# Optimization experiments

Measured on AMD Instinct MI355X. Metric: run time of the kernel, lower is better.

Reference implementation:

```python
import jax, jax.numpy as jnp
import numpy as np

D, L, C, H, W = 4, 16, 64, 128, 128


def setup_inputs() -> dict:
    key = jax.random.key(0)
    ks = jax.random.split(key, 20)
    rn = lambda k, shape, s=0.02: jax.random.normal(k, shape, dtype=jnp.float32) * s
    return {
        "x": jax.random.normal(ks[0], (L, C, H, W), dtype=jnp.float32),
        "ln1_g": jnp.ones((D, C, H, W), jnp.float32),
        "ln1_b": jnp.zeros((D, C, H, W), jnp.float32),
        "Wq": rn(ks[1], (D, C, C)), "bq": jnp.zeros((D, C), jnp.float32),
        "Wk": rn(ks[2], (D, C, C)), "bk": jnp.zeros((D, C), jnp.float32),
        "Wv": rn(ks[3], (D, C, C)), "bv": jnp.zeros((D, C), jnp.float32),
        "Wa": rn(ks[4], (D, 1, 2 * C, 5, 5)), "ba": jnp.zeros((D, 1), jnp.float32),
        "ln2_g": jnp.ones((D, C, H, W), jnp.float32),
        "ln2_b": jnp.zeros((D, C, H, W), jnp.float32),
        "W1": rn(ks[5], (D, 2 * C, C)), "b1": jnp.zeros((D, 2 * C), jnp.float32),
        "W2": rn(ks[6], (D, C, 2 * C)), "b2": jnp.zeros((D, C), jnp.float32),
    }


def _layernorm(x, g, b):
    # torch nn.LayerNorm([C,H,W]): normalize over last 3 dims per frame, eps=1e-5
    mu = jnp.mean(x, axis=(1, 2, 3), keepdims=True)
    var = jnp.var(x, axis=(1, 2, 3), keepdims=True)
    return (x - mu) * jax.lax.rsqrt(var + 1e-5) * g[None] + b[None]


def _conv5(x, w):
    # x: [L, Cin, H, W], w: [1, Cin, 5, 5] -> [L, 1, H, W], SAME padding (pad=2)
    return jax.lax.conv_general_dilated(
        x, w, window_strides=(1, 1), padding="SAME",
        dimension_numbers=("NCHW", "OIHW", "NCHW"))


def _conv1x1(x, w, b):
    # 1x1 conv == per-pixel linear over channels
    return jnp.einsum("lchw,oc->lohw", x, w) + b[None, :, None, None]


def reference(x, ln1_g, ln1_b, Wq, bq, Wk, bk, Wv, bv, Wa, ba,
              ln2_g, ln2_b, W1, b1, W2, b2):
    depth = ln1_g.shape[0]
    c = Wa.shape[2] // 2
    for d in range(depth):
        # --- pre-norm conv attention (nheads=1) + residual ---
        h = _layernorm(x, ln1_g[d], ln1_b[d])
        Q = _conv1x1(h, Wq[d], bq[d])
        K = _conv1x1(h, Wk[d], bk[d])
        V = _conv1x1(h, Wv[d], bv[d])
        # conv_atten(cat([Q_i, K_j])) is linear in channels: split the 5x5
        # kernel into Q-part and K-part, so H_ij = A_i + B_j + bias.
        A = _conv5(Q, Wa[d, :, :c])[:, 0]   # [L, H, W]
        B = _conv5(K, Wa[d, :, c:])[:, 0]   # [L, H, W]
        S = A[:, None] + B[None, :] + ba[d][0]      # [L, L, H, W]
        P = jax.nn.softmax(S, axis=1)               # softmax over source frames j
        attn = jnp.einsum("ijhw,jchw->ichw", P, V)  # weighted sum of V_j
        x = x + attn
        # --- pre-norm conv FFN + residual ---
        h = _layernorm(x, ln2_g[d], ln2_b[d])
        f = _conv1x1(h, W1[d], b1[d])
        f = jax.nn.leaky_relu(f, 0.01)  # torch LeakyReLU default slope
        f = _conv1x1(f, W2[d], b2[d])
        x = x + f
    return x
```

## Files before the change

### kernel.cpp

```cpp
#include <hip/hip_runtime.h>


#define HW 16384
#define CHW 1048576
#define NB 64

typedef unsigned short u16;
typedef __attribute__((ext_vector_type(8))) short bf16x8;
typedef __attribute__((ext_vector_type(8))) unsigned short u16x8;
typedef __attribute__((ext_vector_type(4))) float f32x4;

static __device__ __forceinline__ u16 f2bf(float f) {
  union { float f; unsigned int u; } v; v.f = f;
  unsigned int r = v.u + 0x7fffu + ((v.u >> 16) & 1u);
  return (u16)(r >> 16);
}
static __device__ __forceinline__ float bf2f(u16 h) {
  union { unsigned int u; float f; } v; v.u = ((unsigned int)h) << 16;
  return v.f;
}
static __device__ __forceinline__ void ln_from_acc_wave(
    const float* acc, int l, int lane, float& mu, float& r) {
  const float invN = 1.f / 1048576.f;
  float2 v = *(const float2*)(acc + lane * 32 + 2 * l);
  float s = v.x, q = v.y;
#pragma unroll
  for (int off = 32; off > 0; off >>= 1) {
    s += __shfl_xor(s, off);
    q += __shfl_xor(q, off);
  }
  mu = s * invN;
  r = rsqrtf(q * invN - mu * mu + 1e-5f);
}

__global__ __launch_bounds__(256) void prep_kernel(
    const float* __restrict__ Wa, const float* __restrict__ Wk,
    const float* __restrict__ Wv, const float* __restrict__ W1,
    const float* __restrict__ W2, u16* __restrict__ w1pk,
    u16* __restrict__ w2pk, u16* __restrict__ wvpk, u16* __restrict__ wepk) {
  int d = blockIdx.x;
  int t = blockIdx.y * 256 + threadIdx.x;
  const int STR = 256 * 16;
  const float* WaK = Wa + ((size_t)d * 128 + 64) * 25;
  const float* Wkd = Wk + d * 4096;
  for (int idx = t; idx < 2048; idx += STR) {
    int frag = idx >> 9, lane = (idx >> 3) & 63, j = idx & 7;
    int mt = frag >> 1, kt = frag & 1;
    int tap = mt * 16 + (lane & 15);
    int ci = kt * 32 + (lane >> 4) * 8 + j;
    float s = 0.f;
    if (tap < 25)
      for (int co = 0; co < 64; ++co)
        s = fmaf(WaK[co * 25 + tap], Wkd[co * 64 + ci], s);
    wepk[d * 2048 + idx] = f2bf(s);
  }
  const float* Wvd = Wv + d * 4096;
  for (int idx = t; idx < 4096; idx += STR) {
    int frag = idx >> 9, lane = (idx >> 3) & 63, j = idx & 7;
    int mt = frag >> 1, kt = frag & 1;
    int co = mt * 16 + (lane & 15);
    int ci = kt * 32 + (lane >> 4) * 8 + j;
    wvpk[d * 4096 + idx] = f2bf(Wvd[co * 64 + ci]);
  }
  const float* W1d = W1 + d * 8192;
  for (int idx = t; idx < 8192; idx += STR) {
    int frag = idx >> 9, lane = (idx >> 3) & 63, j = idx & 7;
    int mt = frag >> 1, kt = frag & 1;
    int o = mt * 16 + (lane & 15);
    int ci = kt * 32 + (lane >> 4) * 8 + j;
    w1pk[d * 8192 + idx] = f2bf(W1d[o * 64 + ci]);
  }
  const float* W2d = W2 + d * 8192;
  for (int idx = t; idx < 8192; idx += STR) {
    int frag = idx >> 9, lane = (idx >> 3) & 63, j = idx & 7;
    int mt2 = frag >> 2, kt2 = frag & 3;
    int c = mt2 * 16 + (lane & 15);
    int o = kt2 * 32 + (lane >> 4) * 8 + j;
    w2pk[d * 8192 + idx] = f2bf(W2d[c * 128 + o]);
  }
}

__global__ __launch_bounds__(256) void lngb_kernel(
    const float* __restrict__ g1, u16* __restrict__ o1) {
  int idx = blockIdx.x * 256 + threadIdx.x;
  float4 v = *(const float4*)(g1 + (size_t)idx * 4);
  ushort4 o;
  o.x = f2bf(v.x); o.y = f2bf(v.y); o.z = f2bf(v.z); o.w = f2bf(v.w);
  *(ushort4*)(o1 + (size_t)idx * 4) = o;
}

__global__ __launch_bounds__(256) void stats_kernel(
    const float* __restrict__ xin, u16* __restrict__ xbf,
    float* __restrict__ acc) {
  int tid = threadIdx.x;
  size_t base = (size_t)blockIdx.x * 4096;
  const float4* in4 = (const float4*)(xin + base);
  float s = 0.f, q = 0.f;
#pragma unroll
  for (int k = 0; k < 4; ++k) {
    float4 v = in4[k * 256 + tid];
    ushort4 o;
    o.x = f2bf(v.x); o.y = f2bf(v.y); o.z = f2bf(v.z); o.w = f2bf(v.w);
    *(ushort4*)(xbf + base + (k * 256 + tid) * 4) = o;
    s += v.x + v.y + v.z + v.w;
    q = fmaf(v.x, v.x, q); q = fmaf(v.y, v.y, q);
    q = fmaf(v.z, v.z, q); q = fmaf(v.w, v.w, q);
  }
#pragma unroll
  for (int off = 32; off > 0; off >>= 1) {
    s += __shfl_down(s, off); q += __shfl_down(q, off);
  }
  __shared__ float ls[4], lq[4];
  int wave = tid >> 6;
  if ((tid & 63) == 0) { ls[wave] = s; lq[wave] = q; }
  __syncthreads();
  if (tid == 0) {
    int frame = blockIdx.x >> 8;
    int bkt = blockIdx.x & (NB - 1);
    atomicAdd(&acc[bkt * 32 + frame * 2], ls[0] + ls[1] + ls[2] + ls[3]);
    atomicAdd(&acc[bkt * 32 + frame * 2 + 1], lq[0] + lq[1] + lq[2] + lq[3]);
  }
}

__global__ __launch_bounds__(256) void tb_kernel(
    const u16* __restrict__ xbf, const u16* __restrict__ g,
    const float* __restrict__ bln, const u16* __restrict__ wep_g,
    const float* __restrict__ accA, float* __restrict__ accBz,
    float* __restrict__ mulr, u16* __restrict__ T) {
  __shared__ __align__(16) char lds[18432];
  u16* hb = (u16*)lds;
  int tid = threadIdx.x;
  int l = blockIdx.y;
  int p0 = blockIdx.x << 7;
  if (blockIdx.x == 0 && blockIdx.y == 0)
    for (int i = tid; i < NB * 32; i += 256) accBz[i] = 0.f;
  int lane = tid & 63;
  float mu, r;
  ln_from_acc_wave(accA, l, lane, mu, r);
  if (blockIdx.x == 0 && tid == 0) {
    mulr[2 * l] = mu;
    mulr[2 * l + 1] = r;
  }

  {
    int pq = tid & 15, cg = tid >> 4;
    int px0 = pq * 8, c0 = cg * 4;
    float vv[4][8];
#pragma unroll
    for (int i = 0; i < 4; ++i) {
      int c = c0 + i;
      size_t gi = (((size_t)l * 64 + c) << 14) + p0 + px0;
      int li = (c << 14) + p0 + px0;
      u16x8 xv = *(const u16x8*)(xbf + gi);
      u16x8 gv = *(const u16x8*)(g + li);
      float4 bb0 = *(const float4*)(bln + li);
      float4 bb1 = *(const float4*)(bln + li + 4);
#pragma unroll
      for (int k = 0; k < 8; ++k) {
        float bbk = k < 4 ? ((const float*)&bb0)[k] : ((const float*)&bb1)[k - 4];
        vv[i][k] = (bf2f(xv[k]) - mu) * r * bf2f(gv[k]) + bbk;
      }
    }
#pragma unroll
    for (int k = 0; k < 8; ++k) {
      int row = px0 + k;
      int col = ((((c0 >> 3) + (row >> 2)) & 7) << 3) | (c0 & 7);
      ushort4 hv;
      hv.x = f2bf(vv[0][k]); hv.y = f2bf(vv[1][k]);
      hv.z = f2bf(vv[2][k]); hv.w = f2bf(vv[3][k]);
      *(ushort4*)(hb + row * 72 + col) = hv;
    }
  }
  __syncthreads();

  int wv = tid >> 6;
  int ln15 = lane & 15, quad = lane >> 4;

  bf16x8 ah[2][2];
#pragma unroll
  for (int mt = 0; mt < 2; ++mt) {
    int px = (wv * 2 + mt) * 16 + ln15;
#pragma unroll
    for (int kt = 0; kt < 2; ++kt) {
      int slot = ((kt * 4 + quad) + (px >> 2)) & 7;
      ah[mt][kt] = *(const bf16x8*)(hb + px * 72 + (slot << 3));
    }
  }
  const bf16x8* weg = (const bf16x8*)wep_g;

  f32x4 accT[2][2];
#pragma unroll
  for (int mt = 0; mt < 2; ++mt)
#pragma unroll
    for (int nt = 0; nt < 2; ++nt) accT[mt][nt] = (f32x4){0.f, 0.f, 0.f, 0.f};
#pragma unroll
  for (int nt = 0; nt < 2; ++nt) {
    bf16x8 b0 = weg[(nt * 2 + 0) * 64 + lane];
    bf16x8 b1w = weg[(nt * 2 + 1) * 64 + lane];
#pragma unroll
    for (int mt = 0; mt < 2; ++mt) {
      accT[mt][nt] = __builtin_amdgcn_mfma_f32_16x16x32_bf16(
          ah[mt][0], b0, accT[mt][nt], 0, 0, 0);
      accT[mt][nt] = __builtin_amdgcn_mfma_f32_16x16x32_bf16(
          ah[mt][1], b1w, accT[mt][nt], 0, 0, 0);
    }
  }

#pragma unroll
  for (int mt = 0; mt < 2; ++mt) {
    int pxb = p0 + (wv * 2 + mt) * 16 + quad * 4;
#pragma unroll
    for (int nt = 0; nt < 2; ++nt) {
      int tap = nt * 16 + ln15;
      if (tap < 25) {
        ushort4 o;
        o.x = f2bf(accT[mt][nt][0]); o.y = f2bf(accT[mt][nt][1]);
        o.z = f2bf(accT[mt][nt][2]); o.w = f2bf(accT[mt][nt][3]);
        *(ushort4*)(T + (((size_t)l * 25 + tap) << 14) + pxb) = o;
      }
    }
  }
}

__global__ __launch_bounds__(256) void bconv_kernel(
    const u16* __restrict__ T, float* __restrict__ B) {
  int gid = blockIdx.x * 256 + threadIdx.x;
  int l = gid >> 14, p = gid & 16383;
  int y = p >> 7, xx = p & 127;
  float s = 0.f;
#pragma unroll
  for (int dy = 0; dy < 5; ++dy) {
    int yy = y + dy - 2;
    if (yy < 0 || yy > 127) continue;
#pragma unroll
    for (int dx = 0; dx < 5; ++dx) {
      int xc = xx + dx - 2;
      if (xc < 0 || xc > 127) continue;
      s += bf2f(T[(((size_t)l * 25 + dy * 5 + dx) << 14) + (yy << 7) + xc]);
    }
  }
  B[gid] = s;
}

__global__ __launch_bounds__(256) void attnc_kernel(
    const u16* __restrict__ xbf, const float* __restrict__ B,
    const u16* __restrict__ g1, const float* __restrict__ b1g,
    const u16* __restrict__ wvp_g, const float* __restrict__ bv,
    const float* __restrict__ mulr, u16* __restrict__ abf,
    float* __restrict__ accB, float* __restrict__ accAz) {
  __shared__ float Prl[16][64];
  __shared__ float scal[64];
  __shared__ __align__(16) u16 hb[64 * 72];
  __shared__ float lsq[4][32];
  int tid = threadIdx.x;
  int p0 = blockIdx.x << 6;
  if (blockIdx.x == 0)
    for (int i = tid; i < NB * 32; i += 256) accAz[i] = 0.f;

  if (tid < 64) {
    float bj[16], m = -1e30f;
#pragma unroll
    for (int j = 0; j < 16; ++j) {
      bj[j] = B[(j << 14) + p0 + tid];
      m = fmaxf(m, bj[j]);
    }
    float sum = 0.f;
#pragma unroll
    for (int j = 0; j < 16; ++j) {
      bj[j] = __expf(bj[j] - m);
      sum += bj[j];
    }
    float inv = 1.f / sum;
    float sc = 0.f;
#pragma unroll
    for (int j = 0; j < 16; ++j) {
      float mu_j = mulr[2 * j], r_j = mulr[2 * j + 1];
      float prl = bj[j] * inv * r_j;
      Prl[j][tid] = prl;
      sc = fmaf(prl, mu_j, sc);
    }
    scal[tid] = sc;
  }
  __syncthreads();

  {
    int c2 = tid >> 3, pxg = tid & 7;
    int px0 = pxg * 8;
    float xbar[2][8];
#pragma unroll
    for (int cc = 0; cc < 2; ++cc)
#pragma unroll
      for (int k = 0; k < 8; ++k) xbar[cc][k] = 0.f;
#pragma unroll
    for (int j = 0; j < 16; ++j) {
      float p8[8];
#pragma unroll
      for (int k = 0; k < 8; ++k) p8[k] = Prl[j][px0 + k];
#pragma unroll
      for (int cc = 0; cc < 2; ++cc) {
        int c = cc * 32 + c2;
        u16x8 xv =
            *(const u16x8*)(xbf + (((size_t)j * 64 + c) << 14) + p0 + px0);
#pragma unroll
        for (int k = 0; k < 8; ++k)
          xbar[cc][k] = fmaf(p8[k], bf2f(xv[k]), xbar[cc][k]);
      }
    }
    float sc8[8];
#pragma unroll
    for (int k = 0; k < 8; ++k) sc8[k] = scal[px0 + k];
#pragma unroll
    for (int cc = 0; cc < 2; ++cc) {
      int c = cc * 32 + c2;
      int li = (c << 14) + p0 + px0;
      u16x8 g8 = *(const u16x8*)(g1 + li);
      float4 b0 = *(const float4*)(b1g + li);
      float4 b1v = *(const float4*)(b1g + li + 4);
#pragma unroll
      for (int k = 0; k < 8; ++k) {
        float bbk = k < 4 ? ((const float*)&b0)[k] : ((const float*)&b1v)[k - 4];
        float hv = bf2f(g8[k]) * (xbar[cc][k] - sc8[k]) + bbk;
        int row = px0 + k;
        int col = ((((c >> 3) + (row >> 2)) & 7) << 3) | (c & 7);
        hb[row * 72 + col] = f2bf(hv);
      }
    }
  }
  __syncthreads();

  int wv = tid >> 6, lane = tid & 63;
  int ln15 = lane & 15, quad = lane >> 4;
  int px = wv * 16 + ln15;
  bf16x8 ah[2];
#pragma unroll
  for (int kt = 0; kt < 2; ++kt) {
    int slot = ((kt * 4 + quad) + (px >> 2)) & 7;
    ah[kt] = *(const bf16x8*)(hb + px * 72 + (slot << 3));
  }
  const bf16x8* wvg = (const bf16x8*)wvp_g;
  f32x4 accV[4];
#pragma unroll
  for (int nt = 0; nt < 4; ++nt) accV[nt] = (f32x4){0.f, 0.f, 0.f, 0.f};
#pragma unroll
  for (int nt = 0; nt < 4; ++nt) {
    bf16x8 b0 = wvg[(nt * 2 + 0) * 64 + lane];
    bf16x8 b1w = wvg[(nt * 2 + 1) * 64 + lane];
    accV[nt] = __builtin_amdgcn_mfma_f32_16x16x32_bf16(ah[0], b0, accV[nt],
                                                       0, 0, 0);
    accV[nt] = __builtin_amdgcn_mfma_f32_16x16x32_bf16(ah[1], b1w, accV[nt],
                                                       0, 0, 0);
  }
  int pxb = p0 + wv * 16 + quad * 4;
  float av[4][4];
#pragma unroll
  for (int nt = 0; nt < 4; ++nt) {
    int c = nt * 16 + ln15;
    float bvc = bv[c];
    ushort4 o;
    av[nt][0] = accV[nt][0] + bvc; o.x = f2bf(av[nt][0]);
    av[nt][1] = accV[nt][1] + bvc; o.y = f2bf(av[nt][1]);
    av[nt][2] = accV[nt][2] + bvc; o.z = f2bf(av[nt][2]);
    av[nt][3] = accV[nt][3] + bvc; o.w = f2bf(av[nt][3]);
    *(ushort4*)(abf + ((size_t)c << 14) + pxb) = o;
  }

  float sf[16], qf[16];
#pragma unroll
  for (int f = 0; f < 16; ++f) {
    float s = 0.f, q = 0.f;
#pragma unroll
    for (int nt = 0; nt < 4; ++nt) {
      int c = nt * 16 + ln15;
      ushort4 xv =
          *(const ushort4*)(xbf + (((size_t)f * 64 + c) << 14) + pxb);
      float v0 = bf2f(xv.x) + av[nt][0], v1 = bf2f(xv.y) + av[nt][1];
      float v2 = bf2f(xv.z) + av[nt][2], v3 = bf2f(xv.w) + av[nt][3];
      s += v0 + v1 + v2 + v3;
      q = fmaf(v0, v0, q); q = fmaf(v1, v1, q);
      q = fmaf(v2, v2, q); q = fmaf(v3, v3, q);
    }
    sf[f] = s; qf[f] = q;
  }
#pragma unroll
  for (int off = 32; off > 0; off >>= 1) {
#pragma unroll
    for (int f = 0; f < 16; ++f) {
      sf[f] += __shfl_down(sf[f], off);
      qf[f] += __shfl_down(qf[f], off);
    }
  }
  if (lane == 0) {
#pragma unroll
    for (int f = 0; f < 16; ++f) {
      lsq[wv][2 * f] = sf[f];
      lsq[wv][2 * f + 1] = qf[f];
    }
  }
  __syncthreads();
  if (tid < 32) {
    int bkt = blockIdx.x & (NB - 1);
    atomicAdd(&accB[bkt * 32 + tid],
              lsq[0][tid] + lsq[1][tid] + lsq[2][tid] + lsq[3][tid]);
  }
}

__global__ __launch_bounds__(256) void ffn_kernel(
    const float* __restrict__ xr, float* __restrict__ xw,
    u16* __restrict__ xbfw, const u16* __restrict__ ap,
    const float* __restrict__ g, const float* __restrict__ bln,
    const u16* __restrict__ w1p_g, const float* __restrict__ b1,
    const u16* __restrict__ w2p_g, const float* __restrict__ b2,
    const float* __restrict__ accB, float* __restrict__ accA, int wrbf) {
  __shared__ __align__(16) char lds[66560];
  float* xaf = (float*)lds;
  u16* hb = (u16*)(lds + 33792);
  u16* f1 = (u16*)(lds + 33792);

  int tid = threadIdx.x;
  int P0 = blockIdx.x << 7;
  int l = P0 >> 14;
  int p0 = P0 & 16383;
  int lane = tid & 63;
  float mu, r;
  ln_from_acc_wave(accB, l, lane, mu, r);

#pragma unroll
  for (int it = 0; it < 2; ++it) {
    int pq = tid & 31, cg = (tid >> 5) + it * 8;
    int px = pq * 4, c0 = cg * 4;
    float vv[4][4];
#pragma unroll
    for (int i = 0; i < 4; ++i) {
      int c = c0 + i;
      size_t gi = (((size_t)l * 64 + c) << 14) + p0 + px;
      int li = (c << 14) + p0 + px;
      float4 xv = *(const float4*)(xr + gi);
      ushort4 av4 = *(const ushort4*)(ap + li);
      float4 gv = *(const float4*)(g + li);
      float4 bb = *(const float4*)(bln + li);
      float4 s4;
      s4.x = xv.x + bf2f(av4.x); s4.y = xv.y + bf2f(av4.y);
      s4.z = xv.z + bf2f(av4.z); s4.w = xv.w + bf2f(av4.w);
      *(float4*)(xaf + c * 132 + px) = s4;
      vv[i][0] = (s4.x - mu) * r * gv.x + bb.x;
      vv[i][1] = (s4.y - mu) * r * gv.y + bb.y;
      vv[i][2] = (s4.z - mu) * r * gv.z + bb.z;
      vv[i][3] = (s4.w - mu) * r * gv.w + bb.w;
    }
#pragma unroll
    for (int k = 0; k < 4; ++k) {
      int row = px + k;
      int col = ((((c0 >> 3) + (row >> 2)) & 7) << 3) | (c0 & 7);
      ushort4 hv;
      hv.x = f2bf(vv[0][k]); hv.y = f2bf(vv[1][k]);
      hv.z = f2bf(vv[2][k]); hv.w = f2bf(vv[3][k]);
      *(ushort4*)(hb + row * 72 + col) = hv;
    }
  }
  __syncthreads();

  int wv = tid >> 6;
  int ln15 = lane & 15, quad = lane >> 4;

  bf16x8 bh[2][2];
#pragma unroll
  for (int nt = 0; nt < 2; ++nt) {
    int px = (wv * 2 + nt) * 16 + ln15;
#pragma unroll
    for (int kt = 0; kt < 2; ++kt) {
      int slot = ((kt * 4 + quad) + (px >> 2)) & 7;
      bh[nt][kt] = *(const bf16x8*)(hb + px * 72 + (slot << 3));
    }
  }
  __syncthreads();

  const bf16x8* w1g = (const bf16x8*)w1p_g;
  const bf16x8* w2g = (const bf16x8*)w2p_g;

#pragma unroll
  for (int mt = 0; mt < 8; ++mt) {
    bf16x8 a1a = w1g[(mt * 2 + 0) * 64 + lane];
    bf16x8 a1b = w1g[(mt * 2 + 1) * 64 + lane];
    f32x4 acc[2];
    acc[0] = (f32x4){0.f, 0.f, 0.f, 0.f};
    acc[1] = (f32x4){0.f, 0.f, 0.f, 0.f};
#pragma unroll
    for (int nt = 0; nt < 2; ++nt) {
      acc[nt] = __builtin_amdgcn_mfma_f32_16x16x32_bf16(a1a, bh[nt][0],
                                                        acc[nt], 0, 0, 0);
      acc[nt] = __builtin_amdgcn_mfma_f32_16x16x32_bf16(a1b, bh[nt][1],
                                                        acc[nt], 0, 0, 0);
    }
    int o0 = mt * 16 + quad * 4;
    float4 b1v = *(const float4*)(b1 + o0);
#pragma unroll
    for (int nt = 0; nt < 2; ++nt) {
      int px = (wv * 2 + nt) * 16 + ln15;
      int swz = (px & 7) * 8;
      float fv[4];
#pragma unroll
      for (int rj = 0; rj < 4; ++rj) {
        float f = acc[nt][rj] + ((const float*)&b1v)[rj];
        fv[rj] = fmaxf(f, 0.01f * f);
      }
      int col = ((o0 & ~7) ^ swz) + (o0 & 7);
      ushort4 ov;
      ov.x = f2bf(fv[0]); ov.y = f2bf(fv[1]);
      ov.z = f2bf(fv[2]); ov.w = f2bf(fv[3]);
      *(ushort4*)(f1 + px * 128 + col) = ov;
    }
  }
  __syncthreads();

  bf16x8 a2[2][4];
#pragma unroll
  for (int mt = 0; mt < 2; ++mt) {
    int px = (wv * 2 + mt) * 16 + ln15;
    int swz = (px & 7) * 8;
#pragma unroll
    for (int kt = 0; kt < 4; ++kt)
      a2[mt][kt] =
          *(const bf16x8*)(f1 + px * 128 + ((kt * 32 + quad * 8) ^ swz));
  }
  f32x4 acc2[2][4];
#pragma unroll
  for (int mt = 0; mt < 2; ++mt)
#pragma unroll
    for (int nt = 0; nt < 4; ++nt) acc2[mt][nt] = (f32x4){0.f, 0.f, 0.f, 0.f};
#pragma unroll
  for (int nt = 0; nt < 4; ++nt) {
    bf16x8 bw[4];
#pragma unroll
    for (int kt = 0; kt < 4; ++kt) bw[kt] = w2g[(nt * 4 + kt) * 64 + lane];
#pragma unroll
    for (int mt = 0; mt < 2; ++mt)
#pragma unroll
      for (int kt = 0; kt < 4; ++kt)
        acc2[mt][nt] = __builtin_amdgcn_mfma_f32_16x16x32_bf16(
            a2[mt][kt], bw[kt], acc2[mt][nt], 0, 0, 0);
  }

  float s = 0.f, q = 0.f;
#pragma unroll
  for (int mt = 0; mt < 2; ++mt) {
    int pxl = (wv * 2 + mt) * 16 + quad * 4;
#pragma unroll
    for (int nt = 0; nt < 4; ++nt) {
      int c = nt * 16 + ln15;
      float b2c = b2[c];
      const float* xac = xaf + c * 132 + pxl;
      float4 v;
      v.x = xac[0] + acc2[mt][nt][0] + b2c;
      v.y = xac[1] + acc2[mt][nt][1] + b2c;
      v.z = xac[2] + acc2[mt][nt][2] + b2c;
      v.w = xac[3] + acc2[mt][nt][3] + b2c;
      size_t gi = (((size_t)l * 64 + c) << 14) + p0 + pxl;
      *(float4*)(xw + gi) = v;
      if (wrbf) {
        ushort4 o;
        o.x = f2bf(v.x); o.y = f2bf(v.y); o.z = f2bf(v.z); o.w = f2bf(v.w);
        *(ushort4*)(xbfw + gi) = o;
      }
      s += v.x + v.y + v.z + v.w;
      q = fmaf(v.x, v.x, q); q = fmaf(v.y, v.y, q);
      q = fmaf(v.z, v.z, q); q = fmaf(v.w, v.w, q);
    }
  }
#pragma unroll
  for (int off = 32; off > 0; off >>= 1) {
    s += __shfl_down(s, off); q += __shfl_down(q, off);
  }
  if (lane == 0) {
    int bkt = blockIdx.x & (NB - 1);
    atomicAdd(&accA[bkt * 32 + l * 2], s);
    atomicAdd(&accA[bkt * 32 + l * 2 + 1], q);
  }
}

extern "C" void kernel_launch(void* const* d_in, const int* in_sizes, int n_in,
                              void* d_out, int out_size, void* d_ws,
                              size_t ws_size, hipStream_t stream) {
  const float* x_in = (const float*)d_in[0];
  const float* ln1_g = (const float*)d_in[1];
  const float* ln1_b = (const float*)d_in[2];
  const float* Wk = (const float*)d_in[5];
  const float* Wv = (const float*)d_in[7];
  const float* bv = (const float*)d_in[8];
  const float* Wa = (const float*)d_in[9];
  const float* ln2_g = (const float*)d_in[11];
  const float* ln2_b = (const float*)d_in[12];
  const float* W1 = (const float*)d_in[13];
  const float* b1 = (const float*)d_in[14];
  const float* W2 = (const float*)d_in[15];
  const float* b2 = (const float*)d_in[16];

  float* xbuf = (float*)d_out;
  char* wsb = (char*)d_ws;
  u16* xbf = (u16*)wsb;
  u16* T = (u16*)(wsb + 33554432);
  u16* abf = (u16*)(wsb + 46661632);
  float* Bbuf = (float*)(wsb + 48758784);
  u16* g1b = (u16*)(wsb + 49807360);
  u16* w1pk = (u16*)(wsb + 58195968);
  u16* w2pk = (u16*)(wsb + 58261504);
  u16* wvpk = (u16*)(wsb + 58327040);
  u16* wepk = (u16*)(wsb + 58359808);
  float* mulr = (float*)(wsb + 58376192);
  float* accA = (float*)(wsb + 58376320);
  float* accB = (float*)(wsb + 58384512);

  hipMemsetAsync(accA, 0, 16384, stream);
  prep_kernel<<<dim3(4, 16), 256, 0, stream>>>(Wa, Wk, Wv, W1, W2, w1pk, w2pk,
                                               wvpk, wepk);
  lngb_kernel<<<4096, 256, 0, stream>>>(ln1_g, g1b);
  stats_kernel<<<4096, 256, 0, stream>>>(x_in, xbf, accA);

  const float* xr = x_in;
  for (int d = 0; d < 4; ++d) {
    tb_kernel<<<dim3(128, 16), 256, 0, stream>>>(
        xbf, g1b + (size_t)d * CHW, ln1_b + (size_t)d * CHW, wepk + d * 2048,
        accA, accB, mulr, T);
    bconv_kernel<<<1024, 256, 0, stream>>>(T, Bbuf);
    attnc_kernel<<<256, 256, 0, stream>>>(
        xbf, Bbuf, g1b + (size_t)d * CHW, ln1_b + (size_t)d * CHW,
        wvpk + d * 4096, bv + d * 64, mulr, abf, accB, accA);
    ffn_kernel<<<2048, 256, 0, stream>>>(
        xr, xbuf, xbf, abf, ln2_g + (size_t)d * CHW, ln2_b + (size_t)d * CHW,
        w1pk + d * 8192, b1 + d * 128, w2pk + d * 8192, b2 + d * 64, accB,
        accA, d < 3 ? 1 : 0);
    xr = xbuf;
  }
}
```

Before: 561.6 us.

## Drop bf16 shadow of x, fuse 5x5 tap-sum into attention, add stats kernel

Removes the bf16 copy of the activations. The tb and attention kernels now read the fp32 x directly, and the FFN no longer writes the bf16 shadow. The separate bconv kernel is folded into the attention kernel, which sums the 25 shifted tap planes into shared memory per block. The attention kernel's in-place LN2 statistics are moved into a new stats2 kernel that streams x plus the attention output. This cuts the bf16 write traffic and one launch, but doubles the bytes of each x read, adds a full pass over x, and moves the tap sum into a 256-block kernel with low parallelism.

```diff
diff --git a/kernel.cpp b/kernel.cpp
--- a/kernel.cpp
+++ b/kernel.cpp
@@ -90,8 +90,7 @@
 }
 
 __global__ __launch_bounds__(256) void stats_kernel(
-    const float* __restrict__ xin, u16* __restrict__ xbf,
-    float* __restrict__ acc) {
+    const float* __restrict__ xin, float* __restrict__ acc) {
   int tid = threadIdx.x;
   size_t base = (size_t)blockIdx.x * 4096;
   const float4* in4 = (const float4*)(xin + base);
@@ -99,9 +98,6 @@
 #pragma unroll
   for (int k = 0; k < 4; ++k) {
     float4 v = in4[k * 256 + tid];
-    ushort4 o;
-    o.x = f2bf(v.x); o.y = f2bf(v.y); o.z = f2bf(v.z); o.w = f2bf(v.w);
-    *(ushort4*)(xbf + base + (k * 256 + tid) * 4) = o;
     s += v.x + v.y + v.z + v.w;
     q = fmaf(v.x, v.x, q); q = fmaf(v.y, v.y, q);
     q = fmaf(v.z, v.z, q); q = fmaf(v.w, v.w, q);
@@ -123,7 +119,7 @@
 }
 
 __global__ __launch_bounds__(256) void tb_kernel(
-    const u16* __restrict__ xbf, const u16* __restrict__ g,
+    const float* __restrict__ x, const u16* __restrict__ g,
     const float* __restrict__ bln, const u16* __restrict__ wep_g,
     const float* __restrict__ accA, float* __restrict__ accBz,
     float* __restrict__ mulr, u16* __restrict__ T) {
@@ -151,14 +147,16 @@
       int c = c0 + i;
       size_t gi = (((size_t)l * 64 + c) << 14) + p0 + px0;
       int li = (c << 14) + p0 + px0;
-      u16x8 xv = *(const u16x8*)(xbf + gi);
+      float4 xv0 = *(const float4*)(x + gi);
+      float4 xv1 = *(const float4*)(x + gi + 4);
       u16x8 gv = *(const u16x8*)(g + li);
       float4 bb0 = *(const float4*)(bln + li);
       float4 bb1 = *(const float4*)(bln + li + 4);
 #pragma unroll
       for (int k = 0; k < 8; ++k) {
+        float xk = k < 4 ? ((const float*)&xv0)[k] : ((const float*)&xv1)[k - 4];
         float bbk = k < 4 ? ((const float*)&bb0)[k] : ((const float*)&bb1)[k - 4];
-        vv[i][k] = (bf2f(xv[k]) - mu) * r * bf2f(gv[k]) + bbk;
+        vv[i][k] = (xk - mu) * r * bf2f(gv[k]) + bbk;
       }
     }
 #pragma unroll
@@ -222,46 +220,47 @@
   }
 }
 
-__global__ __launch_bounds__(256) void bconv_kernel(
-    const u16* __restrict__ T, float* __restrict__ B) {
-  int gid = blockIdx.x * 256 + threadIdx.x;
-  int l = gid >> 14, p = gid & 16383;
-  int y = p >> 7, xx = p & 127;
-  float s = 0.f;
-#pragma unroll
-  for (int dy = 0; dy < 5; ++dy) {
-    int yy = y + dy - 2;
-    if (yy < 0 || yy > 127) continue;
-#pragma unroll
-    for (int dx = 0; dx < 5; ++dx) {
-      int xc = xx + dx - 2;
-      if (xc < 0 || xc > 127) continue;
-      s += bf2f(T[(((size_t)l * 25 + dy * 5 + dx) << 14) + (yy << 7) + xc]);
-    }
-  }
-  B[gid] = s;
-}
-
 __global__ __launch_bounds__(256) void attnc_kernel(
-    const u16* __restrict__ xbf, const float* __restrict__ B,
+    const float* __restrict__ x, const u16* __restrict__ T,
     const u16* __restrict__ g1, const float* __restrict__ b1g,
     const u16* __restrict__ wvp_g, const float* __restrict__ bv,
-    const float* __restrict__ mulr, u16* __restrict__ abf,
-    float* __restrict__ accB, float* __restrict__ accAz) {
+    const float* __restrict__ mulr, u16* __restrict__ abf) {
+  __shared__ float Bsm[16][68];
   __shared__ float Prl[16][64];
   __shared__ float scal[64];
   __shared__ __align__(16) u16 hb[64 * 72];
-  __shared__ float lsq[4][32];
   int tid = threadIdx.x;
   int p0 = blockIdx.x << 6;
-  if (blockIdx.x == 0)
-    for (int i = tid; i < NB * 32; i += 256) accAz[i] = 0.f;
+
+  {
+    int j = tid >> 4, xg = tid & 15;
+    int y0 = p0 >> 7, x0 = p0 & 127;
+    float acc4[4] = {0.f, 0.f, 0.f, 0.f};
+    const u16* Tj = T + (((size_t)j * 25) << 14);
+#pragma unroll
+    for (int dy = 0; dy < 5; ++dy) {
+      int yy = y0 + dy - 2;
+      if (yy < 0 || yy > 127) continue;
+#pragma unroll
+      for (int dx = 0; dx < 5; ++dx) {
+        const u16* Tt = Tj + ((dy * 5 + dx) << 14) + (yy << 7);
+#pragma unroll
+        for (int k = 0; k < 4; ++k) {
+          int xc = x0 + xg * 4 + k + dx - 2;
+          if (xc >= 0 && xc < 128) acc4[k] += bf2f(Tt[xc]);
+        }
+      }
+    }
+#pragma unroll
+    for (int k = 0; k < 4; ++k) Bsm[j][xg * 4 + k] = acc4[k];
+  }
+  __syncthreads();
 
   if (tid < 64) {
     float bj[16], m = -1e30f;
 #pragma unroll
     for (int j = 0; j < 16; ++j) {
-      bj[j] = B[(j << 14) + p0 + tid];
+      bj[j] = Bsm[j][tid];
       m = fmaxf(m, bj[j]);
     }
     float sum = 0.f;
@@ -299,11 +298,15 @@
 #pragma unroll
       for (int cc = 0; cc < 2; ++cc) {
         int c = cc * 32 + c2;
-        u16x8 xv =
-            *(const u16x8*)(xbf + (((size_t)j * 64 + c) << 14) + p0 + px0);
-#pragma unroll
-        for (int k = 0; k < 8; ++k)
-          xbar[cc][k] = fmaf(p8[k], bf2f(xv[k]), xbar[cc][k]);
+        const float* xp = x + (((size_t)j * 64 + c) << 14) + p0 + px0;
+        float4 xv0 = *(const float4*)xp;
+        float4 xv1 = *(const float4*)(xp + 4);
+#pragma unroll
+        for (int k = 0; k < 8; ++k) {
+          float xk =
+              k < 4 ? ((const float*)&xv0)[k] : ((const float*)&xv1)[k - 4];
+          xbar[cc][k] = fmaf(p8[k], xk, xbar[cc][k]);
+        }
       }
     }
     float sc8[8];
@@ -351,66 +354,62 @@
                                                        0, 0, 0);
   }
   int pxb = p0 + wv * 16 + quad * 4;
-  float av[4][4];
 #pragma unroll
   for (int nt = 0; nt < 4; ++nt) {
     int c = nt * 16 + ln15;
     float bvc = bv[c];
     ushort4 o;
-    av[nt][0] = accV[nt][0] + bvc; o.x = f2bf(av[nt][0]);
-    av[nt][1] = accV[nt][1] + bvc; o.y = f2bf(av[nt][1]);
-    av[nt][2] = accV[nt][2] + bvc; o.z = f2bf(av[nt][2]);
-    av[nt][3] = accV[nt][3] + bvc; o.w = f2bf(av[nt][3]);
+    o.x = f2bf(accV[nt][0] + bvc);
+    o.y = f2bf(accV[nt][1] + bvc);
+    o.z = f2bf(accV[nt][2] + bvc);
+    o.w = f2bf(accV[nt][3] + bvc);
     *(ushort4*)(abf + ((size_t)c << 14) + pxb) = o;
   }
-
-  float sf[16], qf[16];
-#pragma unroll
-  for (int f = 0; f < 16; ++f) {
-    float s = 0.f, q = 0.f;
-#pragma unroll
-    for (int nt = 0; nt < 4; ++nt) {
-      int c = nt * 16 + ln15;
-      ushort4 xv =
-          *(const ushort4*)(xbf + (((size_t)f * 64 + c) << 14) + pxb);
-      float v0 = bf2f(xv.x) + av[nt][0], v1 = bf2f(xv.y) + av[nt][1];
-      float v2 = bf2f(xv.z) + av[nt][2], v3 = bf2f(xv.w) + av[nt][3];
-      s += v0 + v1 + v2 + v3;
-      q = fmaf(v0, v0, q); q = fmaf(v1, v1, q);
-      q = fmaf(v2, v2, q); q = fmaf(v3, v3, q);
-    }
-    sf[f] = s; qf[f] = q;
+}
+
+__global__ __launch_bounds__(256) void stats2_kernel(
+    const float* __restrict__ x, const u16* __restrict__ abf,
+    float* __restrict__ accB, float* __restrict__ accAz) {
+  int tid = threadIdx.x;
+  if (blockIdx.x == 0)
+    for (int i = tid; i < NB * 32; i += 256) accAz[i] = 0.f;
+  size_t base = (size_t)blockIdx.x * 4096;
+  int intra = (blockIdx.x & 255) * 4096;
+  float s = 0.f, q = 0.f;
+#pragma unroll
+  for (int k = 0; k < 4; ++k) {
+    int off = (k * 256 + tid) * 4;
+    float4 v = *(const float4*)(x + base + off);
+    ushort4 a4 = *(const ushort4*)(abf + intra + off);
+    float v0 = v.x + bf2f(a4.x), v1 = v.y + bf2f(a4.y);
+    float v2 = v.z + bf2f(a4.z), v3 = v.w + bf2f(a4.w);
+    s += v0 + v1 + v2 + v3;
+    q = fmaf(v0, v0, q); q = fmaf(v1, v1, q);
+    q = fmaf(v2, v2, q); q = fmaf(v3, v3, q);
   }
 #pragma unroll
   for (int off = 32; off > 0; off >>= 1) {
-#pragma unroll
-    for (int f = 0; f < 16; ++f) {
-      sf[f] += __shfl_down(sf[f], off);
-      qf[f] += __shfl_down(qf[f], off);
-    }
-  }
-  if (lane == 0) {
-#pragma unroll
-    for (int f = 0; f < 16; ++f) {
-      lsq[wv][2 * f] = sf[f];
-      lsq[wv][2 * f + 1] = qf[f];
-    }
-  }
-  __syncthreads();
-  if (tid < 32) {
+    s += __shfl_down(s, off); q += __shfl_down(q, off);
+  }
+  __shared__ float ls[4], lq[4];
+  int wave = tid >> 6;
+  if ((tid & 63) == 0) { ls[wave] = s; lq[wave] = q; }
+  __syncthreads();
+  if (tid == 0) {
+    int frame = blockIdx.x >> 8;
     int bkt = blockIdx.x & (NB - 1);
-    atomicAdd(&accB[bkt * 32 + tid],
-              lsq[0][tid] + lsq[1][tid] + lsq[2][tid] + lsq[3][tid]);
+    atomicAdd(&accB[bkt * 32 + frame * 2], ls[0] + ls[1] + ls[2] + ls[3]);
+    atomicAdd(&accB[bkt * 32 + frame * 2 + 1], lq[0] + lq[1] + lq[2] + lq[3]);
   }
 }
 
 __global__ __launch_bounds__(256) void ffn_kernel(
     const float* __restrict__ xr, float* __restrict__ xw,
-    u16* __restrict__ xbfw, const u16* __restrict__ ap,
-    const float* __restrict__ g, const float* __restrict__ bln,
-    const u16* __restrict__ w1p_g, const float* __restrict__ b1,
-    const u16* __restrict__ w2p_g, const float* __restrict__ b2,
-    const float* __restrict__ accB, float* __restrict__ accA, int wrbf) {
+    const u16* __restrict__ ap, const float* __restrict__ g,
+    const float* __restrict__ bln, const u16* __restrict__ w1p_g,
+    const float* __restrict__ b1, const u16* __restrict__ w2p_g,
+    const float* __restrict__ b2, const float* __restrict__ accB,
+    float* __restrict__ accA) {
   __shared__ __align__(16) char lds[66560];
   float* xaf = (float*)lds;
   u16* hb = (u16*)(lds + 33792);
@@ -554,13 +553,7 @@
       v.y = xac[1] + acc2[mt][nt][1] + b2c;
       v.z = xac[2] + acc2[mt][nt][2] + b2c;
       v.w = xac[3] + acc2[mt][nt][3] + b2c;
-      size_t gi = (((size_t)l * 64 + c) << 14) + p0 + pxl;
-      *(float4*)(xw + gi) = v;
-      if (wrbf) {
-        ushort4 o;
-        o.x = f2bf(v.x); o.y = f2bf(v.y); o.z = f2bf(v.z); o.w = f2bf(v.w);
-        *(ushort4*)(xbfw + gi) = o;
-      }
+      *(float4*)(xw + (((size_t)l * 64 + c) << 14) + p0 + pxl) = v;
       s += v.x + v.y + v.z + v.w;
       q = fmaf(v.x, v.x, q); q = fmaf(v.y, v.y, q);
       q = fmaf(v.z, v.z, q); q = fmaf(v.w, v.w, q);
@@ -596,38 +589,36 @@
 
   float* xbuf = (float*)d_out;
   char* wsb = (char*)d_ws;
-  u16* xbf = (u16*)wsb;
-  u16* T = (u16*)(wsb + 33554432);
-  u16* abf = (u16*)(wsb + 46661632);
-  float* Bbuf = (float*)(wsb + 48758784);
-  u16* g1b = (u16*)(wsb + 49807360);
-  u16* w1pk = (u16*)(wsb + 58195968);
-  u16* w2pk = (u16*)(wsb + 58261504);
-  u16* wvpk = (u16*)(wsb + 58327040);
-  u16* wepk = (u16*)(wsb + 58359808);
-  float* mulr = (float*)(wsb + 58376192);
-  float* accA = (float*)(wsb + 58376320);
-  float* accB = (float*)(wsb + 58384512);
+  u16* T = (u16*)wsb;
+  u16* abf = (u16*)(wsb + 13107200);
+  u16* g1b = (u16*)(wsb + 15204352);
+  u16* w1pk = (u16*)(wsb + 23592960);
+  u16* w2pk = (u16*)(wsb + 23658496);
+  u16* wvpk = (u16*)(wsb + 23724032);
+  u16* wepk = (u16*)(wsb + 23756800);
+  float* mulr = (float*)(wsb + 23773184);
+  float* accA = (float*)(wsb + 23773312);
+  float* accB = (float*)(wsb + 23781504);
 
   hipMemsetAsync(accA, 0, 16384, stream);
   prep_kernel<<<dim3(4, 16), 256, 0, stream>>>(Wa, Wk, Wv, W1, W2, w1pk, w2pk,
                                                wvpk, wepk);
   lngb_kernel<<<4096, 256, 0, stream>>>(ln1_g, g1b);
-  stats_kernel<<<4096, 256, 0, stream>>>(x_in, xbf, accA);
+  stats_kernel<<<4096, 256, 0, stream>>>(x_in, accA);
 
   const float* xr = x_in;
   for (int d = 0; d < 4; ++d) {
     tb_kernel<<<dim3(128, 16), 256, 0, stream>>>(
-        xbf, g1b + (size_t)d * CHW, ln1_b + (size_t)d * CHW, wepk + d * 2048,
+        xr, g1b + (size_t)d * CHW, ln1_b + (size_t)d * CHW, wepk + d * 2048,
         accA, accB, mulr, T);
-    bconv_kernel<<<1024, 256, 0, stream>>>(T, Bbuf);
     attnc_kernel<<<256, 256, 0, stream>>>(
-        xbf, Bbuf, g1b + (size_t)d * CHW, ln1_b + (size_t)d * CHW,
-        wvpk + d * 4096, bv + d * 64, mulr, abf, accB, accA);
+        xr, T, g1b + (size_t)d * CHW, ln1_b + (size_t)d * CHW,
+        wvpk + d * 4096, bv + d * 64, mulr, abf);
+    stats2_kernel<<<4096, 256, 0, stream>>>(xr, abf, accB, accA);
     ffn_kernel<<<2048, 256, 0, stream>>>(
-        xr, xbuf, xbf, abf, ln2_g + (size_t)d * CHW, ln2_b + (size_t)d * CHW,
+        xr, xbuf, abf, ln2_g + (size_t)d * CHW, ln2_b + (size_t)d * CHW,
         w1pk + d * 8192, b1 + d * 128, w2pk + d * 8192, b2 + d * 64, accB,
-        accA, d < 3 ? 1 : 0);
+        accA);
     xr = xbuf;
   }
 }
```

Result: no change. 569.7 us (+1.4%).

## Fuse 5x5 B-conv into attention kernel and store LN params as bf16

Applied to the files above, without the earlier changes.

Removes the separate bconv kernel: each attention block now sums the 25 tap planes of T directly into a shared-memory tile of B before the softmax, which drops a launch and the float B round-trip through global memory. Separately, ln1_b, ln2_g and ln2_b are converted to bf16 once up front, alongside ln1_g, so the per-layer LN kernels read half the bytes for gamma and beta. The cost is extra upfront conversion traffic and a 64-pixel-row conv gather inside attnc with fewer blocks (256) doing it. Rounding beta and ln2 gamma to bf16 also adds precision loss.

```diff
diff --git a/kernel.cpp b/kernel.cpp
--- a/kernel.cpp
+++ b/kernel.cpp
@@ -81,12 +81,23 @@
 }
 
 __global__ __launch_bounds__(256) void lngb_kernel(
-    const float* __restrict__ g1, u16* __restrict__ o1) {
+    const float* __restrict__ g1, const float* __restrict__ b1,
+    const float* __restrict__ g2, const float* __restrict__ b2,
+    u16* __restrict__ o1, u16* __restrict__ o2, u16* __restrict__ o3,
+    u16* __restrict__ o4) {
   int idx = blockIdx.x * 256 + threadIdx.x;
-  float4 v = *(const float4*)(g1 + (size_t)idx * 4);
+  const float* src;
+  u16* dst;
+  switch (blockIdx.y) {
+    case 0: src = g1; dst = o1; break;
+    case 1: src = b1; dst = o2; break;
+    case 2: src = g2; dst = o3; break;
+    default: src = b2; dst = o4; break;
+  }
+  float4 v = *(const float4*)(src + (size_t)idx * 4);
   ushort4 o;
   o.x = f2bf(v.x); o.y = f2bf(v.y); o.z = f2bf(v.z); o.w = f2bf(v.w);
-  *(ushort4*)(o1 + (size_t)idx * 4) = o;
+  *(ushort4*)(dst + (size_t)idx * 4) = o;
 }
 
 __global__ __launch_bounds__(256) void stats_kernel(
@@ -124,7 +135,7 @@
 
 __global__ __launch_bounds__(256) void tb_kernel(
     const u16* __restrict__ xbf, const u16* __restrict__ g,
-    const float* __restrict__ bln, const u16* __restrict__ wep_g,
+    const u16* __restrict__ bln, const u16* __restrict__ wep_g,
     const float* __restrict__ accA, float* __restrict__ accBz,
     float* __restrict__ mulr, u16* __restrict__ T) {
   __shared__ __align__(16) char lds[18432];
@@ -153,13 +164,10 @@
       int li = (c << 14) + p0 + px0;
       u16x8 xv = *(const u16x8*)(xbf + gi);
       u16x8 gv = *(const u16x8*)(g + li);
-      float4 bb0 = *(const float4*)(bln + li);
-      float4 bb1 = *(const float4*)(bln + li + 4);
-#pragma unroll
-      for (int k = 0; k < 8; ++k) {
-        float bbk = k < 4 ? ((const float*)&bb0)[k] : ((const float*)&bb1)[k - 4];
-        vv[i][k] = (bf2f(xv[k]) - mu) * r * bf2f(gv[k]) + bbk;
-      }
+      u16x8 b8 = *(const u16x8*)(bln + li);
+#pragma unroll
+      for (int k = 0; k < 8; ++k)
+        vv[i][k] = (bf2f(xv[k]) - mu) * r * bf2f(gv[k]) + bf2f(b8[k]);
     }
 #pragma unroll
     for (int k = 0; k < 8; ++k) {
@@ -222,32 +230,13 @@
   }
 }
 
-__global__ __launch_bounds__(256) void bconv_kernel(
-    const u16* __restrict__ T, float* __restrict__ B) {
-  int gid = blockIdx.x * 256 + threadIdx.x;
-  int l = gid >> 14, p = gid & 16383;
-  int y = p >> 7, xx = p & 127;
-  float s = 0.f;
-#pragma unroll
-  for (int dy = 0; dy < 5; ++dy) {
-    int yy = y + dy - 2;
-    if (yy < 0 || yy > 127) continue;
-#pragma unroll
-    for (int dx = 0; dx < 5; ++dx) {
-      int xc = xx + dx - 2;
-      if (xc < 0 || xc > 127) continue;
-      s += bf2f(T[(((size_t)l * 25 + dy * 5 + dx) << 14) + (yy << 7) + xc]);
-    }
-  }
-  B[gid] = s;
-}
-
 __global__ __launch_bounds__(256) void attnc_kernel(
-    const u16* __restrict__ xbf, const float* __restrict__ B,
-    const u16* __restrict__ g1, const float* __restrict__ b1g,
+    const u16* __restrict__ xbf, const u16* __restrict__ T,
+    const u16* __restrict__ g1, const u16* __restrict__ b1g,
     const u16* __restrict__ wvp_g, const float* __restrict__ bv,
     const float* __restrict__ mulr, u16* __restrict__ abf,
     float* __restrict__ accB, float* __restrict__ accAz) {
+  __shared__ float Bsm[16][68];
   __shared__ float Prl[16][64];
   __shared__ float scal[64];
   __shared__ __align__(16) u16 hb[64 * 72];
@@ -257,11 +246,35 @@
   if (blockIdx.x == 0)
     for (int i = tid; i < NB * 32; i += 256) accAz[i] = 0.f;
 
+  {
+    int j = tid >> 4, xg = tid & 15;
+    int y0 = p0 >> 7, x0 = p0 & 127;
+    float acc4[4] = {0.f, 0.f, 0.f, 0.f};
+    const u16* Tj = T + (((size_t)j * 25) << 14);
+#pragma unroll
+    for (int dy = 0; dy < 5; ++dy) {
+      int yy = y0 + dy - 2;
+      if (yy < 0 || yy > 127) continue;
+#pragma unroll
+      for (int dx = 0; dx < 5; ++dx) {
+        const u16* Tt = Tj + ((dy * 5 + dx) << 14) + (yy << 7);
+#pragma unroll
+        for (int k = 0; k < 4; ++k) {
+          int xc = x0 + xg * 4 + k + dx - 2;
+          if (xc >= 0 && xc < 128) acc4[k] += bf2f(Tt[xc]);
+        }
+      }
+    }
+#pragma unroll
+    for (int k = 0; k < 4; ++k) Bsm[j][xg * 4 + k] = acc4[k];
+  }
+  __syncthreads();
+
   if (tid < 64) {
     float bj[16], m = -1e30f;
 #pragma unroll
     for (int j = 0; j < 16; ++j) {
-      bj[j] = B[(j << 14) + p0 + tid];
+      bj[j] = Bsm[j][tid];
       m = fmaxf(m, bj[j]);
     }
     float sum = 0.f;
@@ -314,12 +327,10 @@
       int c = cc * 32 + c2;
       int li = (c << 14) + p0 + px0;
       u16x8 g8 = *(const u16x8*)(g1 + li);
-      float4 b0 = *(const float4*)(b1g + li);
-      float4 b1v = *(const float4*)(b1g + li + 4);
+      u16x8 b8 = *(const u16x8*)(b1g + li);
 #pragma unroll
       for (int k = 0; k < 8; ++k) {
-        float bbk = k < 4 ? ((const float*)&b0)[k] : ((const float*)&b1v)[k - 4];
-        float hv = bf2f(g8[k]) * (xbar[cc][k] - sc8[k]) + bbk;
+        float hv = bf2f(g8[k]) * (xbar[cc][k] - sc8[k]) + bf2f(b8[k]);
         int row = px0 + k;
         int col = ((((c >> 3) + (row >> 2)) & 7) << 3) | (c & 7);
         hb[row * 72 + col] = f2bf(hv);
@@ -407,7 +418,7 @@
 __global__ __launch_bounds__(256) void ffn_kernel(
     const float* __restrict__ xr, float* __restrict__ xw,
     u16* __restrict__ xbfw, const u16* __restrict__ ap,
-    const float* __restrict__ g, const float* __restrict__ bln,
+    const u16* __restrict__ g, const u16* __restrict__ bln,
     const u16* __restrict__ w1p_g, const float* __restrict__ b1,
     const u16* __restrict__ w2p_g, const float* __restrict__ b2,
     const float* __restrict__ accB, float* __restrict__ accA, int wrbf) {
@@ -436,16 +447,16 @@
       int li = (c << 14) + p0 + px;
       float4 xv = *(const float4*)(xr + gi);
       ushort4 av4 = *(const ushort4*)(ap + li);
-      float4 gv = *(const float4*)(g + li);
-      float4 bb = *(const float4*)(bln + li);
+      ushort4 gv4 = *(const ushort4*)(g + li);
+      ushort4 bb4 = *(const ushort4*)(bln + li);
       float4 s4;
       s4.x = xv.x + bf2f(av4.x); s4.y = xv.y + bf2f(av4.y);
       s4.z = xv.z + bf2f(av4.z); s4.w = xv.w + bf2f(av4.w);
       *(float4*)(xaf + c * 132 + px) = s4;
-      vv[i][0] = (s4.x - mu) * r * gv.x + bb.x;
-      vv[i][1] = (s4.y - mu) * r * gv.y + bb.y;
-      vv[i][2] = (s4.z - mu) * r * gv.z + bb.z;
-      vv[i][3] = (s4.w - mu) * r * gv.w + bb.w;
+      vv[i][0] = (s4.x - mu) * r * bf2f(gv4.x) + bf2f(bb4.x);
+      vv[i][1] = (s4.y - mu) * r * bf2f(gv4.y) + bf2f(bb4.y);
+      vv[i][2] = (s4.z - mu) * r * bf2f(gv4.z) + bf2f(bb4.z);
+      vv[i][3] = (s4.w - mu) * r * bf2f(gv4.w) + bf2f(bb4.w);
     }
 #pragma unroll
     for (int k = 0; k < 4; ++k) {
@@ -599,33 +610,35 @@
   u16* xbf = (u16*)wsb;
   u16* T = (u16*)(wsb + 33554432);
   u16* abf = (u16*)(wsb + 46661632);
-  float* Bbuf = (float*)(wsb + 48758784);
-  u16* g1b = (u16*)(wsb + 49807360);
-  u16* w1pk = (u16*)(wsb + 58195968);
-  u16* w2pk = (u16*)(wsb + 58261504);
-  u16* wvpk = (u16*)(wsb + 58327040);
-  u16* wepk = (u16*)(wsb + 58359808);
-  float* mulr = (float*)(wsb + 58376192);
-  float* accA = (float*)(wsb + 58376320);
-  float* accB = (float*)(wsb + 58384512);
+  u16* g1b = (u16*)(wsb + 48758784);
+  u16* b1b = (u16*)(wsb + 57147392);
+  u16* g2b = (u16*)(wsb + 65536000);
+  u16* b2b = (u16*)(wsb + 73924608);
+  u16* w1pk = (u16*)(wsb + 82313216);
+  u16* w2pk = (u16*)(wsb + 82378752);
+  u16* wvpk = (u16*)(wsb + 82444288);
+  u16* wepk = (u16*)(wsb + 82477056);
+  float* mulr = (float*)(wsb + 82493440);
+  float* accA = (float*)(wsb + 82493568);
+  float* accB = (float*)(wsb + 82501760);
 
   hipMemsetAsync(accA, 0, 16384, stream);
   prep_kernel<<<dim3(4, 16), 256, 0, stream>>>(Wa, Wk, Wv, W1, W2, w1pk, w2pk,
                                                wvpk, wepk);
-  lngb_kernel<<<4096, 256, 0, stream>>>(ln1_g, g1b);
+  lngb_kernel<<<dim3(4096, 4), 256, 0, stream>>>(ln1_g, ln1_b, ln2_g, ln2_b,
+                                                 g1b, b1b, g2b, b2b);
   stats_kernel<<<4096, 256, 0, stream>>>(x_in, xbf, accA);
 
   const float* xr = x_in;
   for (int d = 0; d < 4; ++d) {
     tb_kernel<<<dim3(128, 16), 256, 0, stream>>>(
-        xbf, g1b + (size_t)d * CHW, ln1_b + (size_t)d * CHW, wepk + d * 2048,
+        xbf, g1b + (size_t)d * CHW, b1b + (size_t)d * CHW, wepk + d * 2048,
         accA, accB, mulr, T);
-    bconv_kernel<<<1024, 256, 0, stream>>>(T, Bbuf);
     attnc_kernel<<<256, 256, 0, stream>>>(
-        xbf, Bbuf, g1b + (size_t)d * CHW, ln1_b + (size_t)d * CHW,
+        xbf, T, g1b + (size_t)d * CHW, b1b + (size_t)d * CHW,
         wvpk + d * 4096, bv + d * 64, mulr, abf, accB, accA);
     ffn_kernel<<<2048, 256, 0, stream>>>(
-        xr, xbuf, xbf, abf, ln2_g + (size_t)d * CHW, ln2_b + (size_t)d * CHW,
+        xr, xbuf, xbf, abf, g2b + (size_t)d * CHW, b2b + (size_t)d * CHW,
         w1pk + d * 8192, b1 + d * 128, w2pk + d * 8192, b2 + d * 64, accB,
         accA, d < 3 ? 1 : 0);
     xr = xbuf;
```

After: 556.7 us. No clear change (-0.9%).
